# Optimization experiments

Hardware: AMD Instinct MI355X
Metric: run time of the kernel (lower is better)

## Reference

```python
import jax, jax.numpy as jnp
import numpy as np

N_NODES = 100000
N_EDGES = 1600000
N_CRYS = 2000
NODE_F = 64
EDGE_F = 41
N_CONV = 3
H_F = 128
EPS = 1e-5


def _seg_mean(v, idx, n):
    s = jax.ops.segment_sum(v, idx, num_segments=n)
    c = jax.ops.segment_sum(jnp.ones((v.shape[0], 1), v.dtype), idx, num_segments=n)
    return s / jnp.maximum(c, 1.0)


def _bn(x, g, b):
    # training-mode batch norm over dim 0, biased variance (torch semantics)
    m = x.mean(axis=0)
    v = x.var(axis=0)
    return (x - m) * jax.lax.rsqrt(v + EPS) * g + b


def setup_inputs() -> dict:
    key = jax.random.key(0)
    ks = jax.random.split(key, 16)
    inp = {}
    inp['node_fea'] = jax.random.randint(ks[0], (N_NODES,), 0, 101)
    inp['edge_fea'] = jax.random.normal(ks[1], (N_EDGES, EDGE_F), dtype=jnp.float32)
    inp['idx1'] = jax.random.randint(ks[2], (N_EDGES,), 0, N_NODES)
    inp['idx2'] = jax.random.randint(ks[3], (N_EDGES,), 0, N_NODES)
    inp['idx3'] = jnp.sort(jax.random.randint(ks[4], (N_NODES,), 0, N_CRYS))
    # parameters
    din = 2 * NODE_F + EDGE_F
    sc = 1.0 / np.sqrt(din)
    inp['emb'] = jax.random.normal(ks[5], (101, NODE_F), dtype=jnp.float32)
    inp['Wf'] = jax.random.uniform(ks[6], (N_CONV, din, 2 * NODE_F), jnp.float32, -sc, sc)
    inp['bf'] = jax.random.uniform(ks[7], (N_CONV, 2 * NODE_F), jnp.float32, -sc, sc)
    inp['g1'] = jnp.ones((N_CONV, 2 * NODE_F), jnp.float32)
    inp['be1'] = jnp.zeros((N_CONV, 2 * NODE_F), jnp.float32)
    inp['g2'] = jnp.ones((N_CONV, NODE_F), jnp.float32)
    inp['be2'] = jnp.zeros((N_CONV, NODE_F), jnp.float32)
    sc2 = 1.0 / np.sqrt(NODE_F)
    inp['Wc'] = jax.random.uniform(ks[8], (NODE_F, H_F), jnp.float32, -sc2, sc2)
    inp['bc'] = jax.random.uniform(ks[9], (H_F,), jnp.float32, -sc2, sc2)
    sc3 = 1.0 / np.sqrt(H_F)
    inp['Wo'] = jax.random.uniform(ks[10], (H_F, 2), jnp.float32, -sc3, sc3)
    inp['bo'] = jax.random.uniform(ks[11], (2,), jnp.float32, -sc3, sc3)
    return inp


def reference(node_fea, edge_fea, idx1, idx2, idx3, emb, Wf, bf, g1, be1, g2, be2, Wc, bc, Wo, bo):
    x = emb[node_fea]                                   # [N, 64]
    for l in range(N_CONV):
        z12 = jnp.concatenate([x[idx1], x[idx2], edge_fea], axis=1)   # [E, 169]
        z12 = _bn(z12 @ Wf[l] + bf[l], g1[l], be1[l])   # [E, 128]
        gate, conv = jnp.split(z12, 2, axis=1)
        msg = jax.nn.sigmoid(gate) * jax.nn.softplus(conv)
        node_new = _bn(_seg_mean(msg, idx1, N_NODES), g2[l], be2[l])
        x = jax.nn.softplus(x + node_new)
    crys = _seg_mean(x, idx3, N_CRYS)                   # [C, 64]
    crys = jax.nn.softplus(crys @ Wc + bc)              # [C, 128]
    return crys @ Wo + bo                               # [C, 2]
```

## Files before the change

### kernel.cpp

```cpp
#include <hip/hip_runtime.h>
#include <hip/hip_bf16.h>


#define NN 100000
#define NE 1600000
#define NC 2000
#define KPAD 176
#define EFW 48
#define EPSB 1e-5f
#define NCH 1000
#define CH 100

typedef _Float16 f16;
typedef _Float16 half8 __attribute__((ext_vector_type(8)));
typedef _Float16 half2v __attribute__((ext_vector_type(2)));
typedef float f32x16 __attribute__((ext_vector_type(16)));

__device__ __forceinline__ f32x16 zero16() {
    f32x16 v;
#pragma unroll
    for (int i = 0; i < 16; i++) v[i] = 0.f;
    return v;
}
__device__ __forceinline__ float fsoftplus(float x) {
    return fmaxf(x, 0.f) + __logf(1.f + __expf(-fabsf(x)));
}
__device__ __forceinline__ float fsigmoid(float x) {
    return __fdividef(1.f, 1.f + __expf(-x));
}

__global__ void k_prep_x(const int* __restrict__ nf, const float* __restrict__ emb,
                         float* __restrict__ xf, f16* __restrict__ x16) {
    for (int idx = blockIdx.x * blockDim.x + threadIdx.x; idx < NN * 64;
         idx += gridDim.x * blockDim.x) {
        int n = idx >> 6, k = idx & 63;
        float v = emb[nf[n] * 64 + k];
        xf[idx] = v;
        x16[idx] = (f16)v;
    }
}

__global__ void k_deg(const int* __restrict__ idx1, const int* __restrict__ idx3,
                      int* deg1, float* cnt3) {
    for (int i = blockIdx.x * blockDim.x + threadIdx.x; i < NE;
         i += gridDim.x * blockDim.x) {
        atomicAdd(&deg1[idx1[i]], 1);
        if (i < NN) atomicAdd(&cnt3[idx3[i]], 1.f);
    }
}

__global__ void k_scan_a(const int* __restrict__ deg, int* __restrict__ csum) {
    int t = blockIdx.x * blockDim.x + threadIdx.x;
    if (t < NCH) {
        int s = 0;
        int base = t * CH;
        for (int i = 0; i < CH; i++) s += deg[base + i];
        csum[t] = s;
    }
}
__global__ void k_scan_b(const int* __restrict__ csum, int* __restrict__ coff) {
    __shared__ int sc[256];
    int t = threadIdx.x;
    int v[4];
    int part = 0;
#pragma unroll
    for (int q = 0; q < 4; q++) {
        int idx = 4 * t + q;
        v[q] = (idx < NCH) ? csum[idx] : 0;
        part += v[q];
    }
    sc[t] = part;
    __syncthreads();
    for (int off = 1; off < 256; off <<= 1) {
        int add = (t >= off) ? sc[t - off] : 0;
        __syncthreads();
        sc[t] += add;
        __syncthreads();
    }
    int run = sc[t] - part;
#pragma unroll
    for (int q = 0; q < 4; q++) {
        int idx = 4 * t + q;
        if (idx < NCH) coff[idx] = run;
        run += v[q];
    }
}
__global__ void k_scan_c(const int* __restrict__ deg, const int* __restrict__ coff,
                         int* __restrict__ rp) {
    int t = blockIdx.x * blockDim.x + threadIdx.x;
    if (t < NCH) {
        int running = coff[t];
        int base = t * CH;
        for (int i = 0; i < CH; i++) {
            rp[base + i] = running;
            running += deg[base + i];
        }
    }
}

__global__ void k_scatter(const int* __restrict__ idx1, const int* __restrict__ idx2,
                          const int* __restrict__ rp1, int* cur1, int* elist1,
                          int* i1r, int* i2r) {
    for (int e = blockIdx.x * blockDim.x + threadIdx.x; e < NE;
         e += gridDim.x * blockDim.x) {
        int n1 = idx1[e];
        int p = rp1[n1] + atomicAdd(&cur1[n1], 1);
        elist1[p] = e;
        i1r[p] = n1;
        i2r[p] = idx2[e];
    }
}

__global__ void k_prep_efg(const float* __restrict__ ef, const int* __restrict__ elist1,
                           f16* __restrict__ ef16p) {
    for (long idx = (long)blockIdx.x * blockDim.x + threadIdx.x; idx < (long)NE * EFW;
         idx += (long)gridDim.x * blockDim.x) {
        long p = idx / EFW;
        int k = (int)(idx - p * EFW);
        int e = elist1[p];
        float v = (k < 41) ? ef[(size_t)e * 41 + k] : 0.f;
        ef16p[idx] = (f16)v;
    }
}

__global__ void k_wt(const float* __restrict__ Wf_l, f16* __restrict__ WT) {
    for (int idx = blockIdx.x * blockDim.x + threadIdx.x; idx < 128 * KPAD;
         idx += gridDim.x * blockDim.x) {
        int col = idx / KPAD, k = idx % KPAD;
        float v = (k < 169) ? Wf_l[k * 128 + col] : 0.f;
        WT[idx] = (f16)v;
    }
}

__global__ __launch_bounds__(256) void k_edge_a(
    const f16* __restrict__ x16, const f16* __restrict__ ef16p,
    const f16* __restrict__ WT, const int* __restrict__ i1r,
    const int* __restrict__ i2r, float* __restrict__ estats,
    half2v* __restrict__ zp) {
    __shared__ float lst[256];
    int tid = threadIdx.x;
    int lane = tid & 63;
    int w = tid >> 6;
    int h = w >> 1, ch = w & 1;
    int c = lane & 31, kg = lane >> 5;

    half8 bfr[2][11];
#pragma unroll
    for (int t = 0; t < 2; t++) {
        int col = 32 * ch + 64 * t + c;
        const f16* bp = WT + col * KPAD + kg * 8;
#pragma unroll
        for (int s = 0; s < 11; s++)
            bfr[t][s] = *reinterpret_cast<const half8*>(bp + s * 16);
    }

    lst[tid] = 0.f;
    __syncthreads();

    float s1[2] = {0.f, 0.f}, s2[2] = {0.f, 0.f};
    const int NT = NE / 64;
    for (int tile = blockIdx.x; tile < NT; tile += gridDim.x) {
        int p0 = tile * 64 + h * 32;
        long p = p0 + c;
        int i1 = i1r[p], i2 = i2r[p];
        f32x16 acc0 = zero16(), acc1 = zero16();
#pragma unroll
        for (int s = 0; s < 4; s++) {
            half8 a = *reinterpret_cast<const half8*>(x16 + (size_t)i1 * 64 + s * 16 + kg * 8);
            acc0 = __builtin_amdgcn_mfma_f32_32x32x16_f16(a, bfr[0][s], acc0, 0, 0, 0);
            acc1 = __builtin_amdgcn_mfma_f32_32x32x16_f16(a, bfr[1][s], acc1, 0, 0, 0);
        }
#pragma unroll
        for (int s = 0; s < 4; s++) {
            half8 a = *reinterpret_cast<const half8*>(x16 + (size_t)i2 * 64 + s * 16 + kg * 8);
            acc0 = __builtin_amdgcn_mfma_f32_32x32x16_f16(a, bfr[0][4 + s], acc0, 0, 0, 0);
            acc1 = __builtin_amdgcn_mfma_f32_32x32x16_f16(a, bfr[1][4 + s], acc1, 0, 0, 0);
        }
#pragma unroll
        for (int s = 0; s < 3; s++) {
            half8 a = *reinterpret_cast<const half8*>(ef16p + p * EFW + s * 16 + kg * 8);
            acc0 = __builtin_amdgcn_mfma_f32_32x32x16_f16(a, bfr[0][8 + s], acc0, 0, 0, 0);
            acc1 = __builtin_amdgcn_mfma_f32_32x32x16_f16(a, bfr[1][8 + s], acc1, 0, 0, 0);
        }
#pragma unroll
        for (int r = 0; r < 16; r++) {
            float v0 = acc0[r], v1 = acc1[r];
            s1[0] += v0; s2[0] += v0 * v0;
            s1[1] += v1; s2[1] += v1 * v1;
            int row = (r & 3) + 8 * (r >> 2) + 4 * kg;
            half2v pr;
            pr[0] = (f16)v0;
            pr[1] = (f16)v1;
            zp[(size_t)(p0 + row) * 64 + 32 * ch + c] = pr;
        }
    }
#pragma unroll
    for (int t = 0; t < 2; t++) {
        s1[t] += __shfl_xor(s1[t], 32, 64);
        s2[t] += __shfl_xor(s2[t], 32, 64);
    }
    if (kg == 0) {
#pragma unroll
        for (int t = 0; t < 2; t++) {
            int col = 32 * ch + 64 * t + c;
            atomicAdd(&lst[col], s1[t]);
            atomicAdd(&lst[128 + col], s2[t]);
        }
    }
    __syncthreads();
    atomicAdd(&estats[tid], lst[tid]);
}

__global__ __launch_bounds__(256) void k_nodered(
    const half2v* __restrict__ zp, const int* __restrict__ rp1,
    const int* __restrict__ deg1, const float* __restrict__ estats,
    const float* __restrict__ g1, const float* __restrict__ be1,
    float* __restrict__ raw_out, float* __restrict__ nstats) {
    __shared__ float sstat[128];
    int tid = threadIdx.x;
    int j = tid & 63, wv = tid >> 6;
    if (tid < 128) sstat[tid] = 0.f;
    __syncthreads();
    float mg = estats[j] * (1.f / NE);
    float vg = estats[128 + j] * (1.f / NE) - mg * mg;
    float ag = g1[j] * rsqrtf(vg + EPSB);
    float bg = be1[j] - mg * ag;
    float mc = estats[64 + j] * (1.f / NE);
    float vc = estats[192 + j] * (1.f / NE) - mc * mc;
    float ac = g1[64 + j] * rsqrtf(vc + EPSB);
    float bc = be1[64 + j] - mc * ac;
    float p1 = 0.f, p2 = 0.f;
    for (int n = blockIdx.x * 4 + wv; n < NN; n += gridDim.x * 4) {
        int st = rp1[n], d = deg1[n];
        float acc = 0.f;
#pragma unroll 4
        for (int q = 0; q < d; q++) {
            half2v z = __builtin_nontemporal_load(&zp[(size_t)(st + q) * 64 + j]);
            float g = fsigmoid((float)z[0] * ag + bg);
            float s = fsoftplus((float)z[1] * ac + bc);
            acc += g * s;
        }
        float raw = acc / fmaxf((float)d, 1.f);
        raw_out[(size_t)n * 64 + j] = raw;
        p1 += raw;
        p2 += raw * raw;
    }
    atomicAdd(&sstat[j], p1);
    atomicAdd(&sstat[64 + j], p2);
    __syncthreads();
    if (tid < 128) atomicAdd(&nstats[tid], sstat[tid]);
}

template <bool LAST>
__global__ __launch_bounds__(256) void k_node_apply(
    const float* __restrict__ raw_in, const float* __restrict__ nstats,
    const float* __restrict__ g2, const float* __restrict__ be2,
    float* __restrict__ xf, f16* __restrict__ x16, const int* __restrict__ idx3,
    float* __restrict__ crsum) {
    for (int idx = blockIdx.x * blockDim.x + threadIdx.x; idx < NN * 64;
         idx += gridDim.x * blockDim.x) {
        int n = idx >> 6, j = idx & 63;
        float m = nstats[j] * (1.f / NN);
        float var = nstats[64 + j] * (1.f / NN) - m * m;
        float rs = rsqrtf(var + EPSB);
        float a = g2[j] * rs;
        float b = be2[j] - m * a;
        float v = fsoftplus(xf[idx] + raw_in[idx] * a + b);
        if (LAST) {
            atomicAdd(&crsum[(size_t)idx3[n] * 64 + j], v);
        } else {
            xf[idx] = v;
            x16[idx] = (f16)v;
        }
    }
}

__global__ __launch_bounds__(128) void k_out(const float* __restrict__ crsum,
                                             const float* __restrict__ cnt3,
                                             const float* __restrict__ Wc,
                                             const float* __restrict__ bcv,
                                             const float* __restrict__ Wo,
                                             const float* __restrict__ bo,
                                             float* __restrict__ out) {
    __shared__ float crym[64];
    __shared__ float red[4];
    int c = blockIdx.x, tid = threadIdx.x;
    if (tid < 64) crym[tid] = crsum[c * 64 + tid] / fmaxf(cnt3[c], 1.f);
    __syncthreads();
    float hv = bcv[tid];
#pragma unroll
    for (int k = 0; k < 64; k++) hv += crym[k] * Wc[k * 128 + tid];
    hv = fsoftplus(hv);
    float o0 = hv * Wo[tid * 2 + 0];
    float o1 = hv * Wo[tid * 2 + 1];
#pragma unroll
    for (int off = 32; off > 0; off >>= 1) {
        o0 += __shfl_down(o0, off, 64);
        o1 += __shfl_down(o1, off, 64);
    }
    int wv = tid >> 6;
    if ((tid & 63) == 0) { red[wv * 2] = o0; red[wv * 2 + 1] = o1; }
    __syncthreads();
    if (tid == 0) {
        out[c * 2 + 0] = red[0] + red[2] + bo[0];
        out[c * 2 + 1] = red[1] + red[3] + bo[1];
    }
}

static inline size_t al256(size_t x) { return (x + 255) & ~(size_t)255; }

extern "C" void kernel_launch(void* const* d_in, const int* in_sizes, int n_in,
                              void* d_out, int out_size, void* d_ws, size_t ws_size,
                              hipStream_t stream) {
    const int* node_fea = (const int*)d_in[0];
    const float* edge_fea = (const float*)d_in[1];
    const int* idx1 = (const int*)d_in[2];
    const int* idx2 = (const int*)d_in[3];
    const int* idx3 = (const int*)d_in[4];
    const float* emb = (const float*)d_in[5];
    const float* Wf = (const float*)d_in[6];
    const float* g1 = (const float*)d_in[8];
    const float* be1 = (const float*)d_in[9];
    const float* g2 = (const float*)d_in[10];
    const float* be2 = (const float*)d_in[11];
    const float* Wc = (const float*)d_in[12];
    const float* bc = (const float*)d_in[13];
    const float* Wo = (const float*)d_in[14];
    const float* bo = (const float*)d_in[15];
    float* out = (float*)d_out;
    unsigned char* ws = (unsigned char*)d_ws;

    size_t off = 0;
    size_t o_xf = off;     off = al256(off + (size_t)NN * 64 * 4);
    size_t o_x16 = off;    off = al256(off + (size_t)NN * 64 * 2);
    size_t o_efp = off;    off = al256(off + (size_t)NE * EFW * 2);
    size_t o_WT = off;     off = al256(off + (size_t)128 * KPAD * 2);
    size_t o_rp1 = off;    off = al256(off + (size_t)NN * 4);
    size_t o_el1 = off;    off = al256(off + (size_t)NE * 4);
    size_t o_i1r = off;    off = al256(off + (size_t)NE * 4);
    size_t o_i2r = off;    off = al256(off + (size_t)NE * 4);
    size_t o_raw = off;    off = al256(off + (size_t)NN * 64 * 4);
    size_t o_deg1 = off;   off = al256(off + (size_t)NN * 4);
    size_t o_cur1 = off;   off = al256(off + (size_t)NN * 4);
    size_t o_cnt3 = off;   off = al256(off + (size_t)NC * 4);
    size_t o_csum = off;   off = al256(off + 1024 * 4);
    size_t o_coff = off;   off = al256(off + 1024 * 4);
    size_t o_crsum = off;  off = al256(off + (size_t)NC * 64 * 4);
    size_t prep_zero_end = off;
    size_t o_estats = off; off = al256(off + 256 * 4);
    size_t o_nstats = off; off = al256(off + 128 * 4);
    size_t layer_zero_end = off;
    size_t o_z = off;      off = al256(off + (size_t)NE * 64 * 4);
    (void)ws_size;

    float* xf = (float*)(ws + o_xf);
    f16* x16 = (f16*)(ws + o_x16);
    f16* ef16p = (f16*)(ws + o_efp);
    f16* WT = (f16*)(ws + o_WT);
    int* rp1 = (int*)(ws + o_rp1);
    int* elist1 = (int*)(ws + o_el1);
    int* i1r = (int*)(ws + o_i1r);
    int* i2r = (int*)(ws + o_i2r);
    float* raw = (float*)(ws + o_raw);
    int* deg1 = (int*)(ws + o_deg1);
    int* cur1 = (int*)(ws + o_cur1);
    float* cnt3 = (float*)(ws + o_cnt3);
    int* csum = (int*)(ws + o_csum);
    int* coff = (int*)(ws + o_coff);
    float* crsum = (float*)(ws + o_crsum);
    float* estats = (float*)(ws + o_estats);
    float* nstats = (float*)(ws + o_nstats);
    half2v* zp = (half2v*)(ws + o_z);

    hipMemsetAsync(ws + o_deg1, 0, prep_zero_end - o_deg1, stream);
    k_prep_x<<<1024, 256, 0, stream>>>(node_fea, emb, xf, x16);
    k_deg<<<2048, 256, 0, stream>>>(idx1, idx3, deg1, cnt3);
    k_scan_a<<<4, 256, 0, stream>>>(deg1, csum);
    k_scan_b<<<1, 256, 0, stream>>>(csum, coff);
    k_scan_c<<<4, 256, 0, stream>>>(deg1, coff, rp1);
    k_scatter<<<2048, 256, 0, stream>>>(idx1, idx2, rp1, cur1, elist1, i1r, i2r);
    k_prep_efg<<<8192, 256, 0, stream>>>(edge_fea, elist1, ef16p);

    for (int l = 0; l < 3; l++) {
        const float* Wf_l = Wf + (size_t)l * 169 * 128;
        hipMemsetAsync(ws + o_estats, 0, layer_zero_end - o_estats, stream);
        k_wt<<<88, 256, 0, stream>>>(Wf_l, WT);
        k_edge_a<<<2048, 256, 0, stream>>>(x16, ef16p, WT, i1r, i2r, estats, zp);
        k_nodered<<<8192, 256, 0, stream>>>(zp, rp1, deg1, estats, g1 + l * 128,
                                            be1 + l * 128, raw, nstats);
        if (l < 2) {
            k_node_apply<false><<<1024, 256, 0, stream>>>(raw, nstats, g2 + l * 64,
                                                          be2 + l * 64, xf, x16,
                                                          idx3, crsum);
        } else {
            k_node_apply<true><<<1024, 256, 0, stream>>>(raw, nstats, g2 + l * 64,
                                                         be2 + l * 64, xf, x16,
                                                         idx3, crsum);
        }
    }
    k_out<<<2000, 128, 0, stream>>>(crsum, cnt3, Wc, bc, Wo, bo, out);
}
```

Measured before the change: 1.939 ms.

## Vectorize node reduction: 16-byte loads, 4 edges per wave in parallel

The per-node reduction kernel now has each lane load 8 halves (4 channels, gate and conv) with a 16-byte nontemporal load. The four 16-lane groups of a wave walk different edges and are combined with cross-lane shuffles, instead of every lane handling one channel over all edges in sequence. This widens memory transactions and exposes more memory parallelism per node. The edge kernel's z stores also become nontemporal, and the grid is halved. The cost is shuffle overhead and idle sub-groups on low-degree nodes.

```diff
diff --git a/kernel.cpp b/kernel.cpp
--- a/kernel.cpp
+++ b/kernel.cpp
@@ -191,7 +191,7 @@
             half2v pr;
             pr[0] = (f16)v0;
             pr[1] = (f16)v1;
-            zp[(size_t)(p0 + row) * 64 + 32 * ch + c] = pr;
+            __builtin_nontemporal_store(pr, &zp[(size_t)(p0 + row) * 64 + 32 * ch + c]);
         }
     }
 #pragma unroll
@@ -212,41 +212,70 @@
 }
 
 __global__ __launch_bounds__(256) void k_nodered(
-    const half2v* __restrict__ zp, const int* __restrict__ rp1,
+    const f16* __restrict__ zph, const int* __restrict__ rp1,
     const int* __restrict__ deg1, const float* __restrict__ estats,
     const float* __restrict__ g1, const float* __restrict__ be1,
     float* __restrict__ raw_out, float* __restrict__ nstats) {
     __shared__ float sstat[128];
     int tid = threadIdx.x;
-    int j = tid & 63, wv = tid >> 6;
+    int lane = tid & 63;
+    int c4 = lane & 15, sub = lane >> 4;
+    int wv = tid >> 6;
     if (tid < 128) sstat[tid] = 0.f;
     __syncthreads();
-    float mg = estats[j] * (1.f / NE);
-    float vg = estats[128 + j] * (1.f / NE) - mg * mg;
-    float ag = g1[j] * rsqrtf(vg + EPSB);
-    float bg = be1[j] - mg * ag;
-    float mc = estats[64 + j] * (1.f / NE);
-    float vc = estats[192 + j] * (1.f / NE) - mc * mc;
-    float ac = g1[64 + j] * rsqrtf(vc + EPSB);
-    float bc = be1[64 + j] - mc * ac;
-    float p1 = 0.f, p2 = 0.f;
+    float ag[4], bg[4], ac[4], bc[4];
+#pragma unroll
+    for (int u = 0; u < 4; u++) {
+        int j = 4 * c4 + u;
+        float mg = estats[j] * (1.f / NE);
+        float vg = estats[128 + j] * (1.f / NE) - mg * mg;
+        ag[u] = g1[j] * rsqrtf(vg + EPSB);
+        bg[u] = be1[j] - mg * ag[u];
+        float mc = estats[64 + j] * (1.f / NE);
+        float vc = estats[192 + j] * (1.f / NE) - mc * mc;
+        ac[u] = g1[64 + j] * rsqrtf(vc + EPSB);
+        bc[u] = be1[64 + j] - mc * ac[u];
+    }
+    float p1[4] = {0.f, 0.f, 0.f, 0.f}, p2[4] = {0.f, 0.f, 0.f, 0.f};
     for (int n = blockIdx.x * 4 + wv; n < NN; n += gridDim.x * 4) {
         int st = rp1[n], d = deg1[n];
-        float acc = 0.f;
-#pragma unroll 4
-        for (int q = 0; q < d; q++) {
-            half2v z = __builtin_nontemporal_load(&zp[(size_t)(st + q) * 64 + j]);
-            float g = fsigmoid((float)z[0] * ag + bg);
-            float s = fsoftplus((float)z[1] * ac + bc);
-            acc += g * s;
-        }
-        float raw = acc / fmaxf((float)d, 1.f);
-        raw_out[(size_t)n * 64 + j] = raw;
-        p1 += raw;
-        p2 += raw * raw;
-    }
-    atomicAdd(&sstat[j], p1);
-    atomicAdd(&sstat[64 + j], p2);
+        float a[4] = {0.f, 0.f, 0.f, 0.f};
+        for (int q = sub; q < d; q += 4) {
+            half8 z = __builtin_nontemporal_load(
+                reinterpret_cast<const half8*>(zph + (size_t)(st + q) * 128 + 8 * c4));
+#pragma unroll
+            for (int u = 0; u < 4; u++) {
+                float g = fsigmoid((float)z[2 * u] * ag[u] + bg[u]);
+                float s = fsoftplus((float)z[2 * u + 1] * ac[u] + bc[u]);
+                a[u] += g * s;
+            }
+        }
+#pragma unroll
+        for (int u = 0; u < 4; u++) {
+            a[u] += __shfl_xor(a[u], 16, 64);
+            a[u] += __shfl_xor(a[u], 32, 64);
+        }
+        if (sub == 0) {
+            float dn = fmaxf((float)d, 1.f);
+            float rr[4];
+#pragma unroll
+            for (int u = 0; u < 4; u++) {
+                rr[u] = __fdividef(a[u], dn);
+                p1[u] += rr[u];
+                p2[u] += rr[u] * rr[u];
+            }
+            float4 r4;
+            r4.x = rr[0]; r4.y = rr[1]; r4.z = rr[2]; r4.w = rr[3];
+            *reinterpret_cast<float4*>(raw_out + (size_t)n * 64 + 4 * c4) = r4;
+        }
+    }
+    if (sub == 0) {
+#pragma unroll
+        for (int u = 0; u < 4; u++) {
+            atomicAdd(&sstat[4 * c4 + u], p1[u]);
+            atomicAdd(&sstat[64 + 4 * c4 + u], p2[u]);
+        }
+    }
     __syncthreads();
     if (tid < 128) atomicAdd(&nstats[tid], sstat[tid]);
 }
@@ -370,6 +399,7 @@
     float* crsum = (float*)(ws + o_crsum);
     float* estats = (float*)(ws + o_estats);
     float* nstats = (float*)(ws + o_nstats);
+    f16* zph = (f16*)(ws + o_z);
     half2v* zp = (half2v*)(ws + o_z);
 
     hipMemsetAsync(ws + o_deg1, 0, prep_zero_end - o_deg1, stream);
@@ -386,7 +416,7 @@
         hipMemsetAsync(ws + o_estats, 0, layer_zero_end - o_estats, stream);
         k_wt<<<88, 256, 0, stream>>>(Wf_l, WT);
         k_edge_a<<<2048, 256, 0, stream>>>(x16, ef16p, WT, i1r, i2r, estats, zp);
-        k_nodered<<<8192, 256, 0, stream>>>(zp, rp1, deg1, estats, g1 + l * 128,
+        k_nodered<<<4096, 256, 0, stream>>>(zph, rp1, deg1, estats, g1 + l * 128,
                                             be1 + l * 128, raw, nstats);
         if (l < 2) {
             k_node_apply<false><<<1024, 256, 0, stream>>>(raw, nstats, g2 + l * 64,
```

Result: faster. 1.593 ms, median of 2 (-17.9%).
